# Optimization experiments

Hardware: AMD Instinct MI355X
Metric: run time of the kernel (lower is better)

Reference implementation:

```python
import itertools
import jax, jax.numpy as jnp
import numpy as np

B, N_TOK, C = 256, 196, 512
NUM_HEADS, KEY_DIM, ATTN_RATIO, RESOLUTION = 8, 32, 4.0, 14
D_V = int(ATTN_RATIO * KEY_DIM)        # 128
DH = D_V * NUM_HEADS                   # 1024
H_QKV = DH + 2 * KEY_DIM * NUM_HEADS   # 1536
SCALE = KEY_DIM ** (-0.5)


def _build_bias_idxs(resolution):
    points = list(itertools.product(range(resolution), range(resolution)))
    attention_offsets = {}
    idxs = []
    for p1 in points:
        for p2 in points:
            offset = (abs(p1[0] - p2[0]), abs(p1[1] - p2[1]))
            if offset not in attention_offsets:
                attention_offsets[offset] = len(attention_offsets)
            idxs.append(attention_offsets[offset])
    n = len(points)
    return np.array(idxs, dtype=np.int64).reshape(n, n), len(attention_offsets)


def setup_inputs() -> dict:
    key = jax.random.key(0)
    ks = jax.random.split(key, 6)
    idxs_np, n_offsets = _build_bias_idxs(RESOLUTION)  # (196,196), 196 offsets
    return {
        "x": jax.random.normal(ks[0], (B, N_TOK, C), dtype=jnp.float32),
        "qkv_w": jax.random.normal(ks[1], (H_QKV, C), dtype=jnp.float32) * (C ** -0.5),
        "qkv_b": jax.random.normal(ks[2], (H_QKV,), dtype=jnp.float32) * 0.01,
        "proj_w": jax.random.normal(ks[3], (C, DH), dtype=jnp.float32) * (DH ** -0.5),
        "proj_b": jax.random.normal(ks[4], (C,), dtype=jnp.float32) * 0.01,
        "attention_biases": jax.random.normal(ks[5], (NUM_HEADS, n_offsets), dtype=jnp.float32) * 0.02,
        "bias_idxs": jnp.asarray(idxs_np),
    }


def reference(x, qkv_w, qkv_b, proj_w, proj_b, attention_biases, bias_idxs):
    Bsz, N, _ = x.shape
    # qkv projection: (B, N, H_QKV) -> (B, heads, N, 2*key_dim + d_v)
    qkv = x @ qkv_w.T + qkv_b
    qkv = qkv.reshape(Bsz, N, NUM_HEADS, -1).transpose(0, 2, 1, 3)
    q = qkv[..., :KEY_DIM]
    k = qkv[..., KEY_DIM:2 * KEY_DIM]
    v = qkv[..., 2 * KEY_DIM:]
    # learned relative-position bias gather: (heads, N, N)
    bias = attention_biases[:, bias_idxs]
    attn = jnp.einsum("bhnd,bhmd->bhnm", q, k) * SCALE + bias
    attn = jax.nn.softmax(attn, axis=-1)
    out = jnp.einsum("bhnm,bhmd->bhnd", attn, v)  # (B, heads, N, d_v)
    out = out.transpose(0, 2, 1, 3).reshape(Bsz, N, DH)
    return out @ proj_w.T + proj_b
```

## Files before the change

kernel.cpp:

```cpp
#include <hip/hip_runtime.h>

typedef __attribute__((ext_vector_type(8))) short bf16x8;
typedef __attribute__((ext_vector_type(4))) float f32x4;
typedef unsigned short u16;
typedef unsigned int   u32;

#define NTOK  196
#define NH    8
#define DVDIM 128
#define CDIM  512
#define DH    1024
#define SCALE2 0.25505654708103197f
#define NEG_BIG -1.0e30f
#define LOG2E 1.4426950408889634f
#define VSTRIDE 200
#define RESCALE_THR 8.0f

__device__ __forceinline__ u16 f2bf(float f) {
  u32 u = __builtin_bit_cast(u32, f);
  u32 r = u + 0x7FFFu + ((u >> 16) & 1u);
  return (u16)(r >> 16);
}

__device__ __forceinline__ u32 cvtpk(float lo, float hi) {
  u32 r;
  asm("v_cvt_pk_bf16_f32 %0, %1, %2" : "=v"(r) : "v"(lo), "v"(hi));
  return r;
}

__device__ __forceinline__ void stage16(const void* g, char* lds_wave_base, int lane) {
#if __has_builtin(__builtin_amdgcn_global_load_lds)
  __builtin_amdgcn_global_load_lds(
      (const __attribute__((address_space(1))) unsigned int*)g,
      (__attribute__((address_space(3))) unsigned int*)lds_wave_base, 16, 0, 0);
#else
  *(uint4*)(lds_wave_base + lane * 16) = *(const uint4*)g;
#endif
}

__global__ __launch_bounds__(256)
void cvt_k(const float* __restrict__ s, u16* __restrict__ d, int n8) {
  int i = blockIdx.x * 256 + threadIdx.x;
  if (i < n8) {
    const float4* sp = (const float4*)s + (size_t)i * 2;
    float4 a = sp[0], b = sp[1];
    uint4 o;
    o.x = (u32)f2bf(a.x) | ((u32)f2bf(a.y) << 16);
    o.y = (u32)f2bf(a.z) | ((u32)f2bf(a.w) << 16);
    o.z = (u32)f2bf(b.x) | ((u32)f2bf(b.y) << 16);
    o.w = (u32)f2bf(b.z) | ((u32)f2bf(b.w) << 16);
    ((uint4*)d)[i] = o;
  }
}

__global__ __launch_bounds__(224)
void biasT_k(const float* __restrict__ ab, const int* __restrict__ bidx,
             float* __restrict__ bT) {
  const int m = threadIdx.x, j = blockIdx.x, h = blockIdx.y;
  float v = NEG_BIG;
  if (j < NTOK && m < NTOK) v = ab[h * NTOK + bidx[m * NTOK + j]] * LOG2E;
  bT[((size_t)h * 256 + j) * 224 + m] = v;
}

template<int K, int NB, int EPI>
__global__ __launch_bounds__(256)
void gemm_k(const u16* __restrict__ A, const u16* __restrict__ W,
            const float* __restrict__ bias,
            u16* __restrict__ q, u16* __restrict__ kk, u16* __restrict__ vT,
            float* __restrict__ out)
{
  __shared__ __align__(16) u16 As[128 * 32];
  __shared__ __align__(16) u16 Bs[128 * 32];
  const int tid  = threadIdx.x;
  const int bid  = blockIdx.x;
  const int xcd  = bid & 7, t = bid >> 3;
  const int bn   = t % NB, bm = xcd * 49 + t / NB;
  const int lane = tid & 63, w = tid >> 6;
  const int c16  = lane & 15, quad = lane >> 4;
  const int wm   = (w >> 1) * 64, wn = (w & 1) * 64;
  f32x4 acc[4][4] = {};

  const u16* Ab = A + (size_t)bm * 128 * K;
  const u16* Wb = W + (size_t)bn * 128 * K;
  char* ldsA = (char*)As + w * 1024;
  char* ldsB = (char*)Bs + w * 1024;

  for (int k0 = 0; k0 < K; k0 += 32) {
    #pragma unroll
    for (int p = 0; p < 2; ++p) {
      const int i = p * 256 + tid;
      const int m = i >> 2, kp = (i & 3) * 8;
      stage16(Ab + (size_t)m * K + k0 + kp, ldsA + p * 4096, lane);
      stage16(Wb + (size_t)m * K + k0 + kp, ldsB + p * 4096, lane);
    }
    __syncthreads();
    bf16x8 af[4], bfr[4];
    #pragma unroll
    for (int mi = 0; mi < 4; ++mi)
      af[mi] = *(const bf16x8*)&As[(wm + mi * 16 + c16) * 32 + quad * 8];
    #pragma unroll
    for (int ni = 0; ni < 4; ++ni)
      bfr[ni] = *(const bf16x8*)&Bs[(wn + ni * 16 + c16) * 32 + quad * 8];
    #pragma unroll
    for (int mi = 0; mi < 4; ++mi)
      #pragma unroll
      for (int ni = 0; ni < 4; ++ni)
        acc[mi][ni] = __builtin_amdgcn_mfma_f32_16x16x32_bf16(af[mi], bfr[ni], acc[mi][ni], 0, 0, 0);
    __syncthreads();
  }

  if (EPI == 0) {
    #pragma unroll
    for (int ni = 0; ni < 4; ++ni) {
      const int gn = bn * 128 + wn + ni * 16 + c16;
      const int h = gn / 192, d = gn - h * 192;
      const float bv = bias[gn];
      #pragma unroll
      for (int mi = 0; mi < 4; ++mi) {
        const int gm0 = bm * 128 + wm + mi * 16 + quad * 4;
        const int bb = gm0 / 196, tok0 = gm0 - bb * 196;
        const size_t bhh = (size_t)bb * 8 + h;
        const float v0 = acc[mi][ni][0] + bv, v1 = acc[mi][ni][1] + bv;
        const float v2 = acc[mi][ni][2] + bv, v3 = acc[mi][ni][3] + bv;
        if (d < 64) {
          u16* dst = (d < 32) ? (q  + (bhh * 196 + tok0) * 32 + d)
                              : (kk + (bhh * 196 + tok0) * 32 + (d - 32));
          dst[0] = f2bf(v0); dst[32] = f2bf(v1); dst[64] = f2bf(v2); dst[96] = f2bf(v3);
        } else {
          ushort4 pk = { f2bf(v0), f2bf(v1), f2bf(v2), f2bf(v3) };
          *(ushort4*)&vT[(bhh * 128 + (d - 64)) * VSTRIDE + tok0] = pk;
        }
      }
    }
  } else {
    #pragma unroll
    for (int ni = 0; ni < 4; ++ni) {
      const int gn = bn * 128 + wn + ni * 16 + c16;
      const float bv = bias[gn];
      #pragma unroll
      for (int mi = 0; mi < 4; ++mi) {
        const int gm0 = bm * 128 + wm + mi * 16 + quad * 4;
        #pragma unroll
        for (int r = 0; r < 4; ++r)
          out[(size_t)(gm0 + r) * CDIM + gn] = acc[mi][ni][r] + bv;
      }
    }
  }
}

__global__ __launch_bounds__(256)
void attn_k(const u16* __restrict__ q, const u16* __restrict__ kk,
            const u16* __restrict__ vT, const float* __restrict__ bT,
            u16* __restrict__ Ob)
{
  __shared__ __align__(16) u16 k_s[64 * 40];
  __shared__ __align__(16) u16 vt_s[128 * 72];
  __shared__ __align__(16) u16 p_s[4 * 16 * 72];

  const int bh = blockIdx.x;
  const int b = bh >> 3, h = bh & 7;
  const int tid = threadIdx.x;
  const int lane = tid & 63, w = tid >> 6;
  const int c16 = lane & 15, quad = lane >> 4;
  const u16* qb = q  + (size_t)bh * (NTOK * 32);
  const u16* kb = kk + (size_t)bh * (NTOK * 32);
  const u16* vb = vT + (size_t)bh * (DVDIM * VSTRIDE);
  const float* bTh = bT + (size_t)h * 256 * 224;
  const int tmax = blockIdx.y ? 6 : 7;

  int qt[2]; bool act[2]; bf16x8 qf[2];
  #pragma unroll
  for (int s = 0; s < 2; ++s) {
    const int ti = w + 4 * s;
    act[s] = (ti < tmax);
    qt[s] = blockIdx.y * 7 + ti;
    const int tok = min(qt[s] * 16 + c16, NTOK - 1);
    qf[s] = *(const bf16x8*)(qb + (size_t)tok * 32 + quad * 8);
  }
  float mx[2] = {NEG_BIG, NEG_BIG}, lsum[2] = {0.f, 0.f};
  f32x4 oacc[2][8] = {};
  const f32x4 zf = {0.f, 0.f, 0.f, 0.f};

  for (int kc = 0; kc < 4; ++kc) {
    {
      const int key = min(kc * 64 + (tid >> 2), NTOK - 1);
      const int part = (tid & 3) * 8;
      *(uint4*)&k_s[(tid >> 2) * 40 + part] = *(const uint4*)(kb + (size_t)key * 32 + part);
    }
    #pragma unroll
    for (int it = 0; it < 4; ++it) {
      const int idx = tid + it * 256;
      const int dv = idx >> 3, kp = (idx & 7) * 8;
      const int col = min(kc * 64 + kp, 192);
      *(uint4*)&vt_s[dv * 72 + kp] = *(const uint4*)(vb + (size_t)dv * VSTRIDE + col);
    }
    __syncthreads();

    #pragma unroll
    for (int s = 0; s < 2; ++s) {
      if (act[s]) {
        f32x4 sc[4];
        #pragma unroll
        for (int nt = 0; nt < 4; ++nt) {
          bf16x8 kf = *(const bf16x8*)&k_s[(nt * 16 + c16) * 40 + quad * 8];
          sc[nt] = __builtin_amdgcn_mfma_f32_16x16x32_bf16(kf, qf[s], zf, 0, 0, 0);
        }
        const int qg = qt[s] * 16 + c16;
        float ntmx[4];
        #pragma unroll
        for (int nt = 0; nt < 4; ++nt) {
          const float* bp = bTh + (size_t)(kc * 64 + nt * 16 + quad * 4) * 224 + qg;
          #pragma unroll
          for (int r = 0; r < 4; ++r)
            sc[nt][r] = sc[nt][r] * SCALE2 + bp[r * 224];
          ntmx[nt] = fmaxf(fmaxf(sc[nt][0], sc[nt][1]), fmaxf(sc[nt][2], sc[nt][3]));
        }
        const float cmx = fmaxf(fmaxf(ntmx[0], ntmx[1]), fmaxf(ntmx[2], ntmx[3]));

        float alpha = 1.0f;
        if (__ballot(cmx > mx[s] + RESCALE_THR)) {
          float rmx = fmaxf(cmx, __shfl_xor(cmx, 16));
          rmx = fmaxf(rmx, __shfl_xor(rmx, 32));
          const float nmx = fmaxf(mx[s], rmx);
          alpha = exp2f(mx[s] - nmx);
          mx[s] = nmx;
          float a4[4];
          #pragma unroll
          for (int r = 0; r < 4; ++r) a4[r] = __shfl(alpha, quad * 4 + r);
          #pragma unroll
          for (int nt = 0; nt < 8; ++nt)
            #pragma unroll
            for (int r = 0; r < 4; ++r) oacc[s][nt][r] *= a4[r];
        }

        const float m = mx[s];
        float csum = 0.f;
        #pragma unroll
        for (int nt = 0; nt < 4; ++nt) {
          const float p0 = exp2f(sc[nt][0] - m), p1 = exp2f(sc[nt][1] - m);
          const float p2 = exp2f(sc[nt][2] - m), p3 = exp2f(sc[nt][3] - m);
          csum += (p0 + p1) + (p2 + p3);
          uint2 pk;
          pk.x = cvtpk(p0, p1);
          pk.y = cvtpk(p2, p3);
          *(uint2*)&p_s[(w * 16 + c16) * 72 + nt * 16 + quad * 4] = pk;
        }
        csum += __shfl_xor(csum, 16);
        csum += __shfl_xor(csum, 32);
        lsum[s] = lsum[s] * alpha + csum;
        #pragma unroll
        for (int ks = 0; ks < 2; ++ks) {
          bf16x8 ap = *(const bf16x8*)&p_s[(w * 16 + c16) * 72 + ks * 32 + quad * 8];
          #pragma unroll
          for (int nt = 0; nt < 8; ++nt) {
            bf16x8 bv = *(const bf16x8*)&vt_s[(nt * 16 + c16) * 72 + ks * 32 + quad * 8];
            oacc[s][nt] = __builtin_amdgcn_mfma_f32_16x16x32_bf16(ap, bv, oacc[s][nt], 0, 0, 0);
          }
        }
      }
    }
    __syncthreads();
  }

  #pragma unroll
  for (int s = 0; s < 2; ++s) {
    if (!act[s]) continue;
    float lr[4];
    #pragma unroll
    for (int r = 0; r < 4; ++r) lr[r] = __shfl(lsum[s], quad * 4 + r);
    #pragma unroll
    for (int r = 0; r < 4; ++r) {
      const int m = qt[s] * 16 + quad * 4 + r;
      if (m < NTOK) {
        const float inv = 1.0f / lr[r];
        #pragma unroll
        for (int nt = 0; nt < 8; ++nt)
          Ob[((size_t)b * NTOK + m) * DH + h * DVDIM + nt * 16 + c16] =
              f2bf(oacc[s][nt][r] * inv);
      }
    }
  }
}

extern "C" void kernel_launch(void* const* d_in, const int* in_sizes, int n_in,
                              void* d_out, int out_size, void* d_ws, size_t ws_size,
                              hipStream_t stream) {
  const float* x      = (const float*)d_in[0];
  const float* qkv_w  = (const float*)d_in[1];
  const float* qkv_b  = (const float*)d_in[2];
  const float* proj_w = (const float*)d_in[3];
  const float* proj_b = (const float*)d_in[4];
  const float* ab     = (const float*)d_in[5];
  const int*   bidx   = (const int*)d_in[6];
  float* out = (float*)d_out;

  char* p = (char*)d_ws;
  u16*   qw  = (u16*)(p);
  u16*   kw  = (u16*)(p + 25690112);
  u16*   vTw = (u16*)(p + 51380224);
  u16*   w1b = (u16*)(p + 156237824);
  u16*   w3b = (u16*)(p + 157810688);
  float* bT  = (float*)(p + 158859264);
  u16*   xb  = (u16*)(p + 160694272);
  u16*   Ob  = (u16*)(p + 160694272);

  cvt_k<<<12544, 256, 0, stream>>>(x,      xb,  3211264);
  cvt_k<<<  384, 256, 0, stream>>>(qkv_w,  w1b,   98304);
  cvt_k<<<  256, 256, 0, stream>>>(proj_w, w3b,   65536);
  biasT_k<<<dim3(256, 8), 224, 0, stream>>>(ab, bidx, bT);

  gemm_k<512, 12, 0><<<4704, 256, 0, stream>>>(xb, w1b, qkv_b, qw, kw, vTw, nullptr);

  attn_k<<<dim3(2048, 2), 256, 0, stream>>>(qw, kw, vTw, bT, Ob);

  gemm_k<1024, 4, 1><<<1568, 256, 0, stream>>>(Ob, w3b, proj_b, nullptr, nullptr, nullptr, out);
}
```

Baseline: 543.5 us.

## Prefetch next K/V chunk into registers and interleave both query tiles' MFMAs

The attention kernel now loads the next key/value chunk from global memory into registers while computing on the current chunk, then commits it to shared memory between barriers. The two query tiles per wave are processed together: the QK MFMAs and PV MFMAs for both tiles are issued back to back so each loaded K/V fragment is reused, and they are wrapped with s_setprio. Inactive tiles are no longer skipped, so some waves do redundant work on clamped rows. The change also adds a launch-bounds occupancy hint of 2 and doubles the P staging buffer. The added prefetch registers may raise register pressure.

```diff
diff --git a/kernel.cpp b/kernel.cpp
--- a/kernel.cpp
+++ b/kernel.cpp
@@ -148,14 +148,14 @@
   }
 }
 
-__global__ __launch_bounds__(256)
+__global__ __launch_bounds__(256, 2)
 void attn_k(const u16* __restrict__ q, const u16* __restrict__ kk,
             const u16* __restrict__ vT, const float* __restrict__ bT,
             u16* __restrict__ Ob)
 {
   __shared__ __align__(16) u16 k_s[64 * 40];
   __shared__ __align__(16) u16 vt_s[128 * 72];
-  __shared__ __align__(16) u16 p_s[4 * 16 * 72];
+  __shared__ __align__(16) u16 p_s[2][4 * 16 * 72];
 
   const int bh = blockIdx.x;
   const int b = bh >> 3, h = bh & 7;
@@ -181,86 +181,121 @@
   f32x4 oacc[2][8] = {};
   const f32x4 zf = {0.f, 0.f, 0.f, 0.f};
 
+  const int st_key_row = tid >> 2;
+  const int st_key_col = (tid & 3) * 8;
+  const int st_dv[4] = { (tid >> 3), 32 + (tid >> 3), 64 + (tid >> 3), 96 + (tid >> 3) };
+  const int st_kp = (tid & 7) * 8;
+
+  uint4 kreg, vreg[4];
+
+  #define ISSUE(kc_) do {                                                     \
+    const int key_ = min((kc_) * 64 + st_key_row, NTOK - 1);                  \
+    kreg = *(const uint4*)(kb + (size_t)key_ * 32 + st_key_col);              \
+    _Pragma("unroll")                                                         \
+    for (int it = 0; it < 4; ++it) {                                          \
+      const int col_ = min((kc_) * 64 + st_kp, 192);                          \
+      vreg[it] = *(const uint4*)(vb + (size_t)st_dv[it] * VSTRIDE + col_);    \
+    }                                                                         \
+  } while (0)
+
+  #define COMMIT() do {                                                       \
+    *(uint4*)&k_s[st_key_row * 40 + st_key_col] = kreg;                       \
+    _Pragma("unroll")                                                         \
+    for (int it = 0; it < 4; ++it)                                            \
+      *(uint4*)&vt_s[st_dv[it] * 72 + st_kp] = vreg[it];                      \
+  } while (0)
+
+  ISSUE(0);
+  COMMIT();
+  __syncthreads();
+
   for (int kc = 0; kc < 4; ++kc) {
-    {
-      const int key = min(kc * 64 + (tid >> 2), NTOK - 1);
-      const int part = (tid & 3) * 8;
-      *(uint4*)&k_s[(tid >> 2) * 40 + part] = *(const uint4*)(kb + (size_t)key * 32 + part);
-    }
-    #pragma unroll
-    for (int it = 0; it < 4; ++it) {
-      const int idx = tid + it * 256;
-      const int dv = idx >> 3, kp = (idx & 7) * 8;
-      const int col = min(kc * 64 + kp, 192);
-      *(uint4*)&vt_s[dv * 72 + kp] = *(const uint4*)(vb + (size_t)dv * VSTRIDE + col);
-    }
-    __syncthreads();
-
+    if (kc < 3) ISSUE(kc + 1);
+
+    bf16x8 kf4[4];
+    #pragma unroll
+    for (int nt = 0; nt < 4; ++nt)
+      kf4[nt] = *(const bf16x8*)&k_s[(nt * 16 + c16) * 40 + quad * 8];
+    f32x4 sc[2][4];
+    __builtin_amdgcn_s_setprio(1);
+    #pragma unroll
+    for (int nt = 0; nt < 4; ++nt) {
+      sc[0][nt] = __builtin_amdgcn_mfma_f32_16x16x32_bf16(kf4[nt], qf[0], zf, 0, 0, 0);
+      sc[1][nt] = __builtin_amdgcn_mfma_f32_16x16x32_bf16(kf4[nt], qf[1], zf, 0, 0, 0);
+    }
+    __builtin_amdgcn_s_setprio(0);
+
+    float alpha2[2];
     #pragma unroll
     for (int s = 0; s < 2; ++s) {
-      if (act[s]) {
-        f32x4 sc[4];
-        #pragma unroll
-        for (int nt = 0; nt < 4; ++nt) {
-          bf16x8 kf = *(const bf16x8*)&k_s[(nt * 16 + c16) * 40 + quad * 8];
-          sc[nt] = __builtin_amdgcn_mfma_f32_16x16x32_bf16(kf, qf[s], zf, 0, 0, 0);
-        }
-        const int qg = qt[s] * 16 + c16;
-        float ntmx[4];
-        #pragma unroll
-        for (int nt = 0; nt < 4; ++nt) {
-          const float* bp = bTh + (size_t)(kc * 64 + nt * 16 + quad * 4) * 224 + qg;
+      const int qg = min(qt[s] * 16 + c16, 223);
+      float ntmx[4];
+      #pragma unroll
+      for (int nt = 0; nt < 4; ++nt) {
+        const float* bp = bTh + (size_t)(kc * 64 + nt * 16 + quad * 4) * 224 + qg;
+        #pragma unroll
+        for (int r = 0; r < 4; ++r)
+          sc[s][nt][r] = sc[s][nt][r] * SCALE2 + bp[r * 224];
+        ntmx[nt] = fmaxf(fmaxf(sc[s][nt][0], sc[s][nt][1]), fmaxf(sc[s][nt][2], sc[s][nt][3]));
+      }
+      const float cmx = fmaxf(fmaxf(ntmx[0], ntmx[1]), fmaxf(ntmx[2], ntmx[3]));
+
+      float alpha = 1.0f;
+      if (__ballot(cmx > mx[s] + RESCALE_THR)) {
+        float rmx = fmaxf(cmx, __shfl_xor(cmx, 16));
+        rmx = fmaxf(rmx, __shfl_xor(rmx, 32));
+        const float nmx = fmaxf(mx[s], rmx);
+        alpha = exp2f(mx[s] - nmx);
+        mx[s] = nmx;
+        float a4[4];
+        #pragma unroll
+        for (int r = 0; r < 4; ++r) a4[r] = __shfl(alpha, quad * 4 + r);
+        #pragma unroll
+        for (int nt = 0; nt < 8; ++nt)
           #pragma unroll
-          for (int r = 0; r < 4; ++r)
-            sc[nt][r] = sc[nt][r] * SCALE2 + bp[r * 224];
-          ntmx[nt] = fmaxf(fmaxf(sc[nt][0], sc[nt][1]), fmaxf(sc[nt][2], sc[nt][3]));
-        }
-        const float cmx = fmaxf(fmaxf(ntmx[0], ntmx[1]), fmaxf(ntmx[2], ntmx[3]));
-
-        float alpha = 1.0f;
-        if (__ballot(cmx > mx[s] + RESCALE_THR)) {
-          float rmx = fmaxf(cmx, __shfl_xor(cmx, 16));
-          rmx = fmaxf(rmx, __shfl_xor(rmx, 32));
-          const float nmx = fmaxf(mx[s], rmx);
-          alpha = exp2f(mx[s] - nmx);
-          mx[s] = nmx;
-          float a4[4];
-          #pragma unroll
-          for (int r = 0; r < 4; ++r) a4[r] = __shfl(alpha, quad * 4 + r);
-          #pragma unroll
-          for (int nt = 0; nt < 8; ++nt)
-            #pragma unroll
-            for (int r = 0; r < 4; ++r) oacc[s][nt][r] *= a4[r];
-        }
-
-        const float m = mx[s];
-        float csum = 0.f;
-        #pragma unroll
-        for (int nt = 0; nt < 4; ++nt) {
-          const float p0 = exp2f(sc[nt][0] - m), p1 = exp2f(sc[nt][1] - m);
-          const float p2 = exp2f(sc[nt][2] - m), p3 = exp2f(sc[nt][3] - m);
-          csum += (p0 + p1) + (p2 + p3);
-          uint2 pk;
-          pk.x = cvtpk(p0, p1);
-          pk.y = cvtpk(p2, p3);
-          *(uint2*)&p_s[(w * 16 + c16) * 72 + nt * 16 + quad * 4] = pk;
-        }
-        csum += __shfl_xor(csum, 16);
-        csum += __shfl_xor(csum, 32);
-        lsum[s] = lsum[s] * alpha + csum;
-        #pragma unroll
-        for (int ks = 0; ks < 2; ++ks) {
-          bf16x8 ap = *(const bf16x8*)&p_s[(w * 16 + c16) * 72 + ks * 32 + quad * 8];
-          #pragma unroll
-          for (int nt = 0; nt < 8; ++nt) {
-            bf16x8 bv = *(const bf16x8*)&vt_s[(nt * 16 + c16) * 72 + ks * 32 + quad * 8];
-            oacc[s][nt] = __builtin_amdgcn_mfma_f32_16x16x32_bf16(ap, bv, oacc[s][nt], 0, 0, 0);
-          }
-        }
-      }
-    }
-    __syncthreads();
-  }
+          for (int r = 0; r < 4; ++r) oacc[s][nt][r] *= a4[r];
+      }
+      alpha2[s] = alpha;
+
+      const float m = mx[s];
+      float csum = 0.f;
+      #pragma unroll
+      for (int nt = 0; nt < 4; ++nt) {
+        const float p0 = exp2f(sc[s][nt][0] - m), p1 = exp2f(sc[s][nt][1] - m);
+        const float p2 = exp2f(sc[s][nt][2] - m), p3 = exp2f(sc[s][nt][3] - m);
+        csum += (p0 + p1) + (p2 + p3);
+        uint2 pk;
+        pk.x = cvtpk(p0, p1);
+        pk.y = cvtpk(p2, p3);
+        *(uint2*)&p_s[s][(w * 16 + c16) * 72 + nt * 16 + quad * 4] = pk;
+      }
+      csum += __shfl_xor(csum, 16);
+      csum += __shfl_xor(csum, 32);
+      lsum[s] = lsum[s] * alpha2[s] + csum;
+    }
+
+    __builtin_amdgcn_s_setprio(1);
+    #pragma unroll
+    for (int ks = 0; ks < 2; ++ks) {
+      bf16x8 ap0 = *(const bf16x8*)&p_s[0][(w * 16 + c16) * 72 + ks * 32 + quad * 8];
+      bf16x8 ap1 = *(const bf16x8*)&p_s[1][(w * 16 + c16) * 72 + ks * 32 + quad * 8];
+      #pragma unroll
+      for (int nt = 0; nt < 8; ++nt) {
+        bf16x8 bv = *(const bf16x8*)&vt_s[(nt * 16 + c16) * 72 + ks * 32 + quad * 8];
+        oacc[0][nt] = __builtin_amdgcn_mfma_f32_16x16x32_bf16(ap0, bv, oacc[0][nt], 0, 0, 0);
+        oacc[1][nt] = __builtin_amdgcn_mfma_f32_16x16x32_bf16(ap1, bv, oacc[1][nt], 0, 0, 0);
+      }
+    }
+    __builtin_amdgcn_s_setprio(0);
+
+    if (kc < 3) {
+      __syncthreads();
+      COMMIT();
+      __syncthreads();
+    }
+  }
+  #undef ISSUE
+  #undef COMMIT
 
   #pragma unroll
   for (int s = 0; s < 2; ++s) {
```

Result: slower. 563.6 us (+3.7%).

## Split attention into four query groups per head, one tile per wave

Applied to the files above, without the earlier changes.

The attention grid goes from two to four query groups per (batch, head). Each wave now handles a single 16-query tile instead of up to two, which removes the per-wave s-loop and halves the accumulator registers. This raises block count and occupancy. The cost is that K/V tiles are loaded into shared memory twice as often overall. It also adds s_setprio hints around the MFMA sections so matrix work gets scheduling priority.

```diff
diff --git a/kernel.cpp b/kernel.cpp
--- a/kernel.cpp
+++ b/kernel.cpp
@@ -166,20 +166,15 @@
   const u16* kb = kk + (size_t)bh * (NTOK * 32);
   const u16* vb = vT + (size_t)bh * (DVDIM * VSTRIDE);
   const float* bTh = bT + (size_t)h * 256 * 224;
-  const int tmax = blockIdx.y ? 6 : 7;
-
-  int qt[2]; bool act[2]; bf16x8 qf[2];
-  #pragma unroll
-  for (int s = 0; s < 2; ++s) {
-    const int ti = w + 4 * s;
-    act[s] = (ti < tmax);
-    qt[s] = blockIdx.y * 7 + ti;
-    const int tok = min(qt[s] * 16 + c16, NTOK - 1);
-    qf[s] = *(const bf16x8*)(qb + (size_t)tok * 32 + quad * 8);
-  }
-  float mx[2] = {NEG_BIG, NEG_BIG}, lsum[2] = {0.f, 0.f};
-  f32x4 oacc[2][8] = {};
+
+  const int ti  = blockIdx.y * 4 + w;
+  const bool act = (ti < 13);
+  const int tok = min(ti * 16 + c16, NTOK - 1);
+  const bf16x8 qf = *(const bf16x8*)(qb + (size_t)tok * 32 + quad * 8);
+  float mx = NEG_BIG, lsum = 0.f;
+  f32x4 oacc[8] = {};
   const f32x4 zf = {0.f, 0.f, 0.f, 0.f};
+  u16* pw = p_s + w * 16 * 72;
 
   for (int kc = 0; kc < 4; ++kc) {
     {
@@ -196,87 +191,88 @@
     }
     __syncthreads();
 
-    #pragma unroll
-    for (int s = 0; s < 2; ++s) {
-      if (act[s]) {
-        f32x4 sc[4];
-        #pragma unroll
-        for (int nt = 0; nt < 4; ++nt) {
-          bf16x8 kf = *(const bf16x8*)&k_s[(nt * 16 + c16) * 40 + quad * 8];
-          sc[nt] = __builtin_amdgcn_mfma_f32_16x16x32_bf16(kf, qf[s], zf, 0, 0, 0);
+    if (act) {
+      f32x4 sc[4];
+      __builtin_amdgcn_s_setprio(1);
+      #pragma unroll
+      for (int nt = 0; nt < 4; ++nt) {
+        bf16x8 kf = *(const bf16x8*)&k_s[(nt * 16 + c16) * 40 + quad * 8];
+        sc[nt] = __builtin_amdgcn_mfma_f32_16x16x32_bf16(kf, qf, zf, 0, 0, 0);
+      }
+      __builtin_amdgcn_s_setprio(0);
+
+      const int qg = min(ti * 16 + c16, 223);
+      float ntmx[4];
+      #pragma unroll
+      for (int nt = 0; nt < 4; ++nt) {
+        const float* bp = bTh + (size_t)(kc * 64 + nt * 16 + quad * 4) * 224 + qg;
+        #pragma unroll
+        for (int r = 0; r < 4; ++r)
+          sc[nt][r] = sc[nt][r] * SCALE2 + bp[r * 224];
+        ntmx[nt] = fmaxf(fmaxf(sc[nt][0], sc[nt][1]), fmaxf(sc[nt][2], sc[nt][3]));
+      }
+      const float cmx = fmaxf(fmaxf(ntmx[0], ntmx[1]), fmaxf(ntmx[2], ntmx[3]));
+
+      float alpha = 1.0f;
+      if (__ballot(cmx > mx + RESCALE_THR)) {
+        float rmx = fmaxf(cmx, __shfl_xor(cmx, 16));
+        rmx = fmaxf(rmx, __shfl_xor(rmx, 32));
+        const float nmx = fmaxf(mx, rmx);
+        alpha = exp2f(mx - nmx);
+        mx = nmx;
+        float a4[4];
+        #pragma unroll
+        for (int r = 0; r < 4; ++r) a4[r] = __shfl(alpha, quad * 4 + r);
+        #pragma unroll
+        for (int nt = 0; nt < 8; ++nt)
+          #pragma unroll
+          for (int r = 0; r < 4; ++r) oacc[nt][r] *= a4[r];
+      }
+
+      const float m = mx;
+      float csum = 0.f;
+      #pragma unroll
+      for (int nt = 0; nt < 4; ++nt) {
+        const float p0 = exp2f(sc[nt][0] - m), p1 = exp2f(sc[nt][1] - m);
+        const float p2 = exp2f(sc[nt][2] - m), p3 = exp2f(sc[nt][3] - m);
+        csum += (p0 + p1) + (p2 + p3);
+        uint2 pk;
+        pk.x = cvtpk(p0, p1);
+        pk.y = cvtpk(p2, p3);
+        *(uint2*)&pw[c16 * 72 + nt * 16 + quad * 4] = pk;
+      }
+      csum += __shfl_xor(csum, 16);
+      csum += __shfl_xor(csum, 32);
+      lsum = lsum * alpha + csum;
+
+      __builtin_amdgcn_s_setprio(1);
+      #pragma unroll
+      for (int ks = 0; ks < 2; ++ks) {
+        bf16x8 ap = *(const bf16x8*)&pw[c16 * 72 + ks * 32 + quad * 8];
+        #pragma unroll
+        for (int nt = 0; nt < 8; ++nt) {
+          bf16x8 bv = *(const bf16x8*)&vt_s[(nt * 16 + c16) * 72 + ks * 32 + quad * 8];
+          oacc[nt] = __builtin_amdgcn_mfma_f32_16x16x32_bf16(ap, bv, oacc[nt], 0, 0, 0);
         }
-        const int qg = qt[s] * 16 + c16;
-        float ntmx[4];
-        #pragma unroll
-        for (int nt = 0; nt < 4; ++nt) {
-          const float* bp = bTh + (size_t)(kc * 64 + nt * 16 + quad * 4) * 224 + qg;
-          #pragma unroll
-          for (int r = 0; r < 4; ++r)
-            sc[nt][r] = sc[nt][r] * SCALE2 + bp[r * 224];
-          ntmx[nt] = fmaxf(fmaxf(sc[nt][0], sc[nt][1]), fmaxf(sc[nt][2], sc[nt][3]));
-        }
-        const float cmx = fmaxf(fmaxf(ntmx[0], ntmx[1]), fmaxf(ntmx[2], ntmx[3]));
-
-        float alpha = 1.0f;
-        if (__ballot(cmx > mx[s] + RESCALE_THR)) {
-          float rmx = fmaxf(cmx, __shfl_xor(cmx, 16));
-          rmx = fmaxf(rmx, __shfl_xor(rmx, 32));
-          const float nmx = fmaxf(mx[s], rmx);
-          alpha = exp2f(mx[s] - nmx);
-          mx[s] = nmx;
-          float a4[4];
-          #pragma unroll
-          for (int r = 0; r < 4; ++r) a4[r] = __shfl(alpha, quad * 4 + r);
-          #pragma unroll
-          for (int nt = 0; nt < 8; ++nt)
-            #pragma unroll
-            for (int r = 0; r < 4; ++r) oacc[s][nt][r] *= a4[r];
-        }
-
-        const float m = mx[s];
-        float csum = 0.f;
-        #pragma unroll
-        for (int nt = 0; nt < 4; ++nt) {
-          const float p0 = exp2f(sc[nt][0] - m), p1 = exp2f(sc[nt][1] - m);
-          const float p2 = exp2f(sc[nt][2] - m), p3 = exp2f(sc[nt][3] - m);
-          csum += (p0 + p1) + (p2 + p3);
-          uint2 pk;
-          pk.x = cvtpk(p0, p1);
-          pk.y = cvtpk(p2, p3);
-          *(uint2*)&p_s[(w * 16 + c16) * 72 + nt * 16 + quad * 4] = pk;
-        }
-        csum += __shfl_xor(csum, 16);
-        csum += __shfl_xor(csum, 32);
-        lsum[s] = lsum[s] * alpha + csum;
-        #pragma unroll
-        for (int ks = 0; ks < 2; ++ks) {
-          bf16x8 ap = *(const bf16x8*)&p_s[(w * 16 + c16) * 72 + ks * 32 + quad * 8];
-          #pragma unroll
-          for (int nt = 0; nt < 8; ++nt) {
-            bf16x8 bv = *(const bf16x8*)&vt_s[(nt * 16 + c16) * 72 + ks * 32 + quad * 8];
-            oacc[s][nt] = __builtin_amdgcn_mfma_f32_16x16x32_bf16(ap, bv, oacc[s][nt], 0, 0, 0);
-          }
-        }
-      }
+      }
+      __builtin_amdgcn_s_setprio(0);
     }
     __syncthreads();
   }
 
-  #pragma unroll
-  for (int s = 0; s < 2; ++s) {
-    if (!act[s]) continue;
+  if (act) {
     float lr[4];
     #pragma unroll
-    for (int r = 0; r < 4; ++r) lr[r] = __shfl(lsum[s], quad * 4 + r);
+    for (int r = 0; r < 4; ++r) lr[r] = __shfl(lsum, quad * 4 + r);
     #pragma unroll
     for (int r = 0; r < 4; ++r) {
-      const int m = qt[s] * 16 + quad * 4 + r;
+      const int m = ti * 16 + quad * 4 + r;
       if (m < NTOK) {
         const float inv = 1.0f / lr[r];
         #pragma unroll
         for (int nt = 0; nt < 8; ++nt)
           Ob[((size_t)b * NTOK + m) * DH + h * DVDIM + nt * 16 + c16] =
-              f2bf(oacc[s][nt][r] * inv);
+              f2bf(oacc[nt][r] * inv);
       }
     }
   }
@@ -311,7 +307,7 @@
 
   gemm_k<512, 12, 0><<<4704, 256, 0, stream>>>(xb, w1b, qkv_b, qw, kw, vTw, nullptr);
 
-  attn_k<<<dim3(2048, 2), 256, 0, stream>>>(qw, kw, vTw, bT, Ob);
+  attn_k<<<dim3(2048, 4), 256, 0, stream>>>(qw, kw, vTw, bT, Ob);
 
   gemm_k<1024, 4, 1><<<1568, 256, 0, stream>>>(Ob, w3b, proj_b, nullptr, nullptr, nullptr, out);
 }
```

Measured after the change: 540.5 us. Within noise of the previous version (-0.6%).
